# Optimization experiments

Hardware: AMD Instinct MI355X
Metric: run time of the kernel (lower is better)

Reference implementation:

```python
import jax, jax.numpy as jnp
import numpy as np

N = 100000          # nodes
E = 1600000         # directed edges
F_IN = 512          # num_features
H = 8               # heads
FH = 8              # per-head out channels
C = H * FH          # 64 hidden channels
HID = (2 * C) // 2  # 64, PyG JK lstm hidden size
NUM_CLASSES = 40
NEG_SLOPE = 0.2     # GATConv leaky relu slope


def setup_inputs() -> dict:
    key = jax.random.key(0)
    ks = jax.random.split(key, 24)
    s = 0.1
    inp = {
        "x": jax.random.normal(ks[0], (N, F_IN), jnp.float32),
        "edge_index": jax.random.randint(ks[1], (2, E), 0, N, jnp.int64)
        if jax.config.jax_enable_x64 else jax.random.randint(ks[1], (2, E), 0, N, jnp.int32),
        # GATConv 1
        "W1": jax.random.normal(ks[2], (F_IN, H * FH), jnp.float32) * s,
        "a1_src": jax.random.normal(ks[3], (H, FH), jnp.float32) * s,
        "a1_dst": jax.random.normal(ks[4], (H, FH), jnp.float32) * s,
        "b1": jnp.zeros((H * FH,), jnp.float32),
        # GATConv 2
        "W2": jax.random.normal(ks[5], (C, H * FH), jnp.float32) * s,
        "a2_src": jax.random.normal(ks[6], (H, FH), jnp.float32) * s,
        "a2_dst": jax.random.normal(ks[7], (H, FH), jnp.float32) * s,
        "b2": jnp.zeros((H * FH,), jnp.float32),
        # JK bidirectional LSTM (torch gate order i,f,g,o)
        "Wih_f": jax.random.normal(ks[8], (4 * HID, C), jnp.float32) * s,
        "Whh_f": jax.random.normal(ks[9], (4 * HID, HID), jnp.float32) * s,
        "bih_f": jnp.zeros((4 * HID,), jnp.float32),
        "bhh_f": jnp.zeros((4 * HID,), jnp.float32),
        "Wih_b": jax.random.normal(ks[10], (4 * HID, C), jnp.float32) * s,
        "Whh_b": jax.random.normal(ks[11], (4 * HID, HID), jnp.float32) * s,
        "bih_b": jnp.zeros((4 * HID,), jnp.float32),
        "bhh_b": jnp.zeros((4 * HID,), jnp.float32),
        # JK attention head
        "w_att": jax.random.normal(ks[12], (2 * HID,), jnp.float32) * s,
        "b_att": jnp.zeros((), jnp.float32),
        # output layer (bias=False)
        "W_out": jax.random.normal(ks[13], (NUM_CLASSES, C), jnp.float32) * s,
    }
    return inp


def gat_layer(x, src, dst, W, a_src, a_dst, b):
    n = x.shape[0]
    h = (x @ W).reshape(n, H, FH)                       # [N,H,FH]
    al_s = jnp.einsum('nhf,hf->nh', h, a_src)           # [N,H]
    al_d = jnp.einsum('nhf,hf->nh', h, a_dst)
    e = jax.nn.leaky_relu(al_s[src] + al_d[dst], NEG_SLOPE)  # [E',H]
    m = jax.ops.segment_max(e, dst, num_segments=n)     # segment softmax over dst
    ex = jnp.exp(e - m[dst])
    ssum = jax.ops.segment_sum(ex, dst, num_segments=n)
    alpha = ex / ssum[dst]                              # [E',H]
    out = jax.ops.segment_sum(h[src] * alpha[:, :, None], dst, num_segments=n)
    return out.reshape(n, H * FH) + b


def lstm_dir(xs, Wih, Whh, bih, bhh):
    # xs: [L, N, C] -> hs: [L, N, HID]
    n = xs.shape[1]

    def step(carry, xt):
        hprev, cprev = carry
        g = xt @ Wih.T + bih + hprev @ Whh.T + bhh
        i, f, gg, o = jnp.split(g, 4, axis=-1)
        c = jax.nn.sigmoid(f) * cprev + jax.nn.sigmoid(i) * jnp.tanh(gg)
        hh = jax.nn.sigmoid(o) * jnp.tanh(c)
        return (hh, c), hh

    init = (jnp.zeros((n, HID), xs.dtype), jnp.zeros((n, HID), xs.dtype))
    _, hs = jax.lax.scan(step, init, xs)
    return hs


def reference(x, edge_index, W1, a1_src, a1_dst, b1, W2, a2_src, a2_dst, b2,
              Wih_f, Whh_f, bih_f, bhh_f, Wih_b, Whh_b, bih_b, bhh_b,
              w_att, b_att, W_out):
    n = x.shape[0]
    loop = jnp.arange(n, dtype=edge_index.dtype)        # PyG add_self_loops
    src = jnp.concatenate([edge_index[0], loop])
    dst = jnp.concatenate([edge_index[1], loop])

    # eval mode: dropouts are identity
    x1 = jax.nn.elu(gat_layer(x, src, dst, W1, a1_src, a1_dst, b1))   # [N,64]
    x2 = gat_layer(x1, src, dst, W2, a2_src, a2_dst, b2)              # [N,64]

    xs = jnp.stack([x1, x2], axis=0)                    # [L=2, N, 64]
    h_f = lstm_dir(xs, Wih_f, Whh_f, bih_f, bhh_f)
    h_b = lstm_dir(xs[::-1], Wih_b, Whh_b, bih_b, bhh_b)[::-1]
    hcat = jnp.concatenate([h_f, h_b], axis=-1)         # [2, N, 128]

    att = jnp.einsum('lnk,k->ln', hcat, w_att) + b_att  # [2, N]
    alpha = jax.nn.softmax(att, axis=0)
    final = jnp.sum(xs * alpha[:, :, None], axis=0)     # [N, 64]

    return jax.nn.log_softmax(final @ W_out.T, axis=-1)
```

## Files before the change

### kernel.cpp

```cpp
#include <hip/hip_runtime.h>
#include <math.h>

#define F_IN 512
#define NCLS 40
#define BSH 7
#define BNODES (1 << BSH)
#define CH 16384

typedef __attribute__((ext_vector_type(8))) short bf16x8;
typedef __attribute__((ext_vector_type(4))) float f32x4;

__device__ __forceinline__ f32x4 mfma_bf16(bf16x8 a, bf16x8 b, f32x4 c){
  return __builtin_amdgcn_mfma_f32_16x16x32_bf16(a, b, c, 0, 0, 0);
}
__device__ __forceinline__ float fsigm(float x){ return 1.f/(1.f+__expf(-x)); }
__device__ __forceinline__ float ftanh(float x){ return 1.f - 2.f/(__expf(2.f*x)+1.f); }
__device__ __forceinline__ unsigned short f2bf(float f){
  unsigned u = __float_as_uint(f);
  return (unsigned short)((u + 0x7fffu + ((u>>16)&1u)) >> 16);
}
__device__ __forceinline__ float bf2f(unsigned short h){
  return __uint_as_float(((unsigned)h) << 16);
}
__device__ __forceinline__ unsigned cvtpk(float lo, float hi){
  unsigned r;
  asm("v_cvt_pk_bf16_f32 %0, %1, %2" : "=v"(r) : "v"(lo), "v"(hi));
  return r;
}

__global__ __launch_bounds__(256) void k_pcount(const int* __restrict__ ei, int e, int n,
                                                int nb, int* __restrict__ bhist){
  __shared__ int h[1024];
  int b = blockIdx.x, t = threadIdx.x;
  for (int i = t; i < nb; i += 256) h[i] = 0;
  __syncthreads();
  int tot = e + n;
  int base = b*CH;
  int lim = min(base + CH, tot);
  for (int i = base + t; i < lim; i += 256){
    int d = (i < e) ? ei[e + i] : (i - e);
    atomicAdd(&h[d >> BSH], 1);
  }
  __syncthreads();
  for (int i = t; i < nb; i += 256) bhist[(size_t)b*nb + i] = h[i];
}

__global__ __launch_bounds__(256) void k_pscan1(int* __restrict__ bhist, int nb, int B,
                                                int* __restrict__ bcnt){
  int i = blockIdx.x*256 + threadIdx.x;
  if (i >= nb) return;
  int run = 0;
  for (int b = 0; b < B; b++){
    int v = bhist[(size_t)b*nb + i];
    bhist[(size_t)b*nb + i] = run;
    run += v;
  }
  bcnt[i] = run;
}

__global__ __launch_bounds__(256) void k_pscan2(const int* __restrict__ bcnt, int nb, int tot,
                                                int* __restrict__ bbase,
                                                int* __restrict__ rowptr, int n){
  __shared__ int sb[256];
  __shared__ int carry;
  int t = threadIdx.x;
  if (t == 0) carry = 0;
  __syncthreads();
  for (int c0 = 0; c0 < nb; c0 += 256){
    int v = (c0 + t < nb) ? bcnt[c0 + t] : 0;
    sb[t] = v; __syncthreads();
    for (int off = 1; off < 256; off <<= 1){
      int u = (t >= off) ? sb[t-off] : 0; __syncthreads();
      sb[t] += u; __syncthreads();
    }
    if (c0 + t < nb) bbase[c0 + t] = carry + sb[t] - v;
    __syncthreads();
    if (t == 0) carry += sb[255];
    __syncthreads();
  }
  if (t == 0){ bbase[nb] = carry; rowptr[n] = tot; }
}

__global__ __launch_bounds__(256) void k_pscatter(const int* __restrict__ ei, int e, int n,
                                                  int nb, const int* __restrict__ bhist,
                                                  const int* __restrict__ bbase,
                                                  unsigned* __restrict__ bedges){
  __shared__ int cur[1024];
  int b = blockIdx.x, t = threadIdx.x;
  for (int i = t; i < nb; i += 256)
    cur[i] = bbase[i] + bhist[(size_t)b*nb + i];
  __syncthreads();
  int tot = e + n;
  int base = b*CH;
  int lim = min(base + CH, tot);
  for (int i = base + t; i < lim; i += 256){
    int s, d;
    if (i < e){ s = ei[i]; d = ei[e + i]; } else { s = i - e; d = s; }
    int pos = atomicAdd(&cur[d >> BSH], 1);
    bedges[pos] = (unsigned)s | ((unsigned)(d & (BNODES-1)) << 20);
  }
}

__global__ __launch_bounds__(256) void k_bbuild(const unsigned* __restrict__ bedges,
                                                const int* __restrict__ bbase,
                                                int* __restrict__ rowptr, int* __restrict__ col, int n){
  int b = blockIdx.x;
  int t = threadIdx.x;
  __shared__ int hist[BNODES];
  __shared__ int sc[BNODES];
  __shared__ int cur[BNODES];
  int beg = bbase[b], end = bbase[b+1];
  if (t < BNODES) hist[t] = 0;
  __syncthreads();
  for (int i = beg + t; i < end; i += 256)
    atomicAdd(&hist[bedges[i] >> 20], 1);
  __syncthreads();
  int v = (t < BNODES) ? hist[t] : 0;
  if (t < BNODES) sc[t] = v;
  __syncthreads();
  for (int off = 1; off < BNODES; off <<= 1){
    int u = (t >= off && t < BNODES) ? sc[t-off] : 0;
    __syncthreads();
    if (t < BNODES) sc[t] += u;
    __syncthreads();
  }
  if (t < BNODES){
    int excl = sc[t] - v;
    int node = (b << BSH) + t;
    if (node < n) rowptr[node] = beg + excl;
    cur[t] = excl;
  }
  __syncthreads();
  for (int i = beg + t; i < end; i += 256){
    unsigned pk = bedges[i];
    int pos = atomicAdd(&cur[pk >> 20], 1);
    col[beg + pos] = (int)(pk & 0xFFFFFu);
  }
}

__global__ __launch_bounds__(256) void k_prep(
    const float* __restrict__ W1, const float* __restrict__ W2,
    const float* __restrict__ Wihf, const float* __restrict__ Whhf,
    const float* __restrict__ Wihb, const float* __restrict__ Whhb,
    unsigned short* __restrict__ W1T, unsigned short* __restrict__ W2T,
    unsigned short* __restrict__ Wfx, unsigned short* __restrict__ Wfh,
    unsigned short* __restrict__ Wbx, unsigned short* __restrict__ Wbh)
{
  int i = blockIdx.x*256 + threadIdx.x;
  if (i < 32768){
    int k = i >> 6, c = i & 63;
    W1T[c*512 + k] = f2bf(W1[i]);
  } else if (i < 36864){
    int j = i - 32768; int k = j >> 6, c = j & 63;
    W2T[c*64 + k] = f2bf(W2[j]);
  } else if (i < 102400){
    int j = i - 36864;
    int which = j >> 14, o = j & 16383;
    const float* src = which==0 ? Wihf : which==1 ? Whhf : which==2 ? Wihb : Whhb;
    unsigned short* dst = which==0 ? Wfx : which==1 ? Wfh : which==2 ? Wbx : Wbh;
    dst[o] = f2bf(src[o]);
  }
}

__global__ __launch_bounds__(256, 2) void k_gemm512(
    const float* __restrict__ Xf, const unsigned short* __restrict__ WT,
    const float* __restrict__ as_, const float* __restrict__ ad_,
    unsigned short* __restrict__ Hb, unsigned short* __restrict__ alsb,
    float* __restrict__ ald, int n)
{
  __shared__ unsigned short xs[64*512];
  int t = threadIdx.x;
  int n0 = blockIdx.x*64;
  char* xsb = reinterpret_cast<char*>(xs);

  bool full = (n0 + 64 <= n);
  #pragma unroll
  for (int i = 0; i < 16; i++){
    int g  = i*256 + t;
    int row = g >> 6;
    int ck  = g & 63;
    const float* src = full ? (Xf + (size_t)(n0 + row)*512 + ck*8)
                            : (Xf + (size_t)min(n0 + row, n-1)*512 + ck*8);
    float4 u0 = reinterpret_cast<const float4*>(src)[0];
    float4 u1 = reinterpret_cast<const float4*>(src)[1];
    uint4 pk;
    pk.x = cvtpk(u0.x, u0.y);
    pk.y = cvtpk(u0.z, u0.w);
    pk.z = cvtpk(u1.x, u1.y);
    pk.w = cvtpk(u1.z, u1.w);
    int byte = row*1024 + ((ck*16) ^ ((row & 7) << 4));
    *reinterpret_cast<uint4*>(xsb + byte) = pk;
  }
  __syncthreads();

  int w = t >> 6, l = t & 63;
  int c = l & 15, kg = l >> 4;
  int row = w*16 + c;
  const unsigned short* wp0 = WT + (size_t)c*512 + kg*8;

  f32x4 acc[4];
  #pragma unroll
  for (int j = 0; j < 4; j++) acc[j] = (f32x4){0.f,0.f,0.f,0.f};

  #pragma unroll
  for (int kt = 0; kt < 16; ++kt){
    int colb = (kt*64 + kg*16) ^ ((row & 7) << 4);
    bf16x8 a = *reinterpret_cast<const bf16x8*>(xsb + row*1024 + colb);
    #pragma unroll
    for (int j = 0; j < 4; j++){
      bf16x8 b = *reinterpret_cast<const bf16x8*>(wp0 + j*8192 + kt*32);
      acc[j] = mfma_bf16(a, b, acc[j]);
    }
  }

  float asl[4], adl[4];
  #pragma unroll
  for (int j = 0; j < 4; j++){ asl[j] = as_[j*16 + c]; adl[j] = ad_[j*16 + c]; }
  #pragma unroll
  for (int j = 0; j < 4; j++){
    #pragma unroll
    for (int r = 0; r < 4; r++){
      int grow = n0 + w*16 + kg*4 + r;
      float v = acc[j][r];
      if (grow < n) Hb[(size_t)grow*64 + j*16 + c] = f2bf(v);
      float sv = v*asl[j];
      float dv = v*adl[j];
      sv += __shfl_xor(sv, 1, 64); sv += __shfl_xor(sv, 2, 64); sv += __shfl_xor(sv, 4, 64);
      dv += __shfl_xor(dv, 1, 64); dv += __shfl_xor(dv, 2, 64); dv += __shfl_xor(dv, 4, 64);
      if ((c & 7) == 0 && grow < n){
        int head = j*2 + (c >> 3);
        alsb[(size_t)grow*8 + head] = f2bf(sv);
        ald [(size_t)grow*8 + head] = dv;
      }
    }
  }
}

__global__ __launch_bounds__(256) void k_gemm64(
    const unsigned short* __restrict__ Xh, const unsigned short* __restrict__ WT,
    const float* __restrict__ as_, const float* __restrict__ ad_,
    unsigned short* __restrict__ Hb, unsigned short* __restrict__ alsb,
    float* __restrict__ ald, int n)
{
  int t = threadIdx.x;
  int w = t >> 6, l = t & 63;
  int c = l & 15, kg = l >> 4;
  int n0 = blockIdx.x*64 + w*16;
  int row = min(n0 + c, n-1);
  f32x4 acc[4];
  #pragma unroll
  for (int j = 0; j < 4; j++) acc[j] = (f32x4){0.f,0.f,0.f,0.f};

  #pragma unroll
  for (int kt = 0; kt < 2; ++kt){
    int ko = kt*32 + kg*8;
    bf16x8 a = *reinterpret_cast<const bf16x8*>(Xh + (size_t)row*64 + ko);
    #pragma unroll
    for (int j = 0; j < 4; j++){
      bf16x8 b = *reinterpret_cast<const bf16x8*>(WT + (size_t)(j*16 + c)*64 + ko);
      acc[j] = mfma_bf16(a, b, acc[j]);
    }
  }
  float asl[4], adl[4];
  #pragma unroll
  for (int j = 0; j < 4; j++){ asl[j] = as_[j*16 + c]; adl[j] = ad_[j*16 + c]; }
  #pragma unroll
  for (int j = 0; j < 4; j++){
    #pragma unroll
    for (int r = 0; r < 4; r++){
      int grow = n0 + kg*4 + r;
      float v = acc[j][r];
      if (grow < n) Hb[(size_t)grow*64 + j*16 + c] = f2bf(v);
      float sv = v*asl[j];
      float dv = v*adl[j];
      sv += __shfl_xor(sv, 1, 64); sv += __shfl_xor(sv, 2, 64); sv += __shfl_xor(sv, 4, 64);
      dv += __shfl_xor(dv, 1, 64); dv += __shfl_xor(dv, 2, 64); dv += __shfl_xor(dv, 4, 64);
      if ((c & 7) == 0 && grow < n){
        int head = j*2 + (c >> 3);
        alsb[(size_t)grow*8 + head] = f2bf(sv);
        ald [(size_t)grow*8 + head] = dv;
      }
    }
  }
}

struct EdgeBuf {
  float a0, a1, a2, a3;
  uint4 h0, h1, h2, h3;
};

__device__ __forceinline__ void loadEB(EdgeBuf& b, const int* __restrict__ col,
                                       int pos, int beg, int end,
                                       const unsigned short* __restrict__ ap,
                                       const unsigned short* __restrict__ Hp){
  int s0 = (pos   < end) ? col[pos]   : col[beg];
  int s1 = (pos+1 < end) ? col[pos+1] : s0;
  int s2 = (pos+2 < end) ? col[pos+2] : s0;
  int s3 = (pos+3 < end) ? col[pos+3] : s0;
  b.a0 = bf2f(ap[s0*8]); b.a1 = bf2f(ap[s1*8]);
  b.a2 = bf2f(ap[s2*8]); b.a3 = bf2f(ap[s3*8]);
  b.h0 = *reinterpret_cast<const uint4*>(Hp + (size_t)s0*64);
  b.h1 = *reinterpret_cast<const uint4*>(Hp + (size_t)s1*64);
  b.h2 = *reinterpret_cast<const uint4*>(Hp + (size_t)s2*64);
  b.h3 = *reinterpret_cast<const uint4*>(Hp + (size_t)s3*64);
}

__device__ __forceinline__ void acc8(float (&acc)[8], float xf, uint4 g){
  acc[0] = fmaf(xf, bf2f((unsigned short)g.x), acc[0]);
  acc[1] = fmaf(xf, bf2f((unsigned short)(g.x>>16)), acc[1]);
  acc[2] = fmaf(xf, bf2f((unsigned short)g.y), acc[2]);
  acc[3] = fmaf(xf, bf2f((unsigned short)(g.y>>16)), acc[3]);
  acc[4] = fmaf(xf, bf2f((unsigned short)g.z), acc[4]);
  acc[5] = fmaf(xf, bf2f((unsigned short)(g.z>>16)), acc[5]);
  acc[6] = fmaf(xf, bf2f((unsigned short)g.w), acc[6]);
  acc[7] = fmaf(xf, bf2f((unsigned short)(g.w>>16)), acc[7]);
}

__device__ __forceinline__ void computeEB(const EdgeBuf& b, int pos, int end, float adv,
                                          float& ssum, float (&acc)[8]){
  float e0 = b.a0 + adv; e0 = (e0>0.f)?e0:0.2f*e0;
  float e1 = b.a1 + adv; e1 = (e1>0.f)?e1:0.2f*e1;
  float e2 = b.a2 + adv; e2 = (e2>0.f)?e2:0.2f*e2;
  float e3 = b.a3 + adv; e3 = (e3>0.f)?e3:0.2f*e3;
  float x0 = __expf(e0);
  float x1 = (pos+1 < end) ? __expf(e1) : 0.f;
  float x2 = (pos+2 < end) ? __expf(e2) : 0.f;
  float x3 = (pos+3 < end) ? __expf(e3) : 0.f;
  ssum += (x0 + x1) + (x2 + x3);
  acc8(acc, x0, b.h0);
  acc8(acc, x1, b.h1);
  acc8(acc, x2, b.h2);
  acc8(acc, x3, b.h3);
}

template<bool DO_ELU>
__global__ __launch_bounds__(256) void k_agg(
    const int* __restrict__ rowptr, const int* __restrict__ col,
    const unsigned short* __restrict__ Hb, const unsigned short* __restrict__ alsb,
    const float* __restrict__ ald, const float* __restrict__ bias,
    unsigned short* __restrict__ outb, int n)
{
  int grp = threadIdx.x >> 3;
  int ln  = threadIdx.x & 7;
  int node = blockIdx.x*32 + grp;
  if (node >= n) return;
  float adv = ald[node*8 + ln];
  int beg = rowptr[node], end = rowptr[node+1];
  const unsigned short* Hp = Hb + ln*8;
  const unsigned short* ap = alsb + ln;

  float acc[8];
  #pragma unroll
  for (int q = 0; q < 8; q++) acc[q] = 0.f;
  float ssum = 0.f;

  EdgeBuf A, B;
  int p = beg;
  loadEB(A, col, p,   beg, end, ap, Hp);
  loadEB(B, col, p+4, beg, end, ap, Hp);
  while (true){
    computeEB(A, p, end, adv, ssum, acc);
    if (p + 8 < end) loadEB(A, col, p+8, beg, end, ap, Hp);
    p += 4;
    if (p >= end) break;
    computeEB(B, p, end, adv, ssum, acc);
    if (p + 8 < end) loadEB(B, col, p+8, beg, end, ap, Hp);
    p += 4;
    if (p >= end) break;
  }

  float inv = 1.f/ssum;
  ushort4 pk0, pk1;
  float o[8];
  #pragma unroll
  for (int q = 0; q < 8; q++){
    o[q] = acc[q]*inv + bias[ln*8 + q];
    if (DO_ELU) o[q] = (o[q] > 0.f) ? o[q] : (__expf(o[q]) - 1.f);
  }
  pk0.x = f2bf(o[0]); pk0.y = f2bf(o[1]); pk0.z = f2bf(o[2]); pk0.w = f2bf(o[3]);
  pk1.x = f2bf(o[4]); pk1.y = f2bf(o[5]); pk1.z = f2bf(o[6]); pk1.w = f2bf(o[7]);
  *reinterpret_cast<ushort4*>(outb + (size_t)node*64 + ln*8)     = pk0;
  *reinterpret_cast<ushort4*>(outb + (size_t)node*64 + ln*8 + 4) = pk1;
}

__global__ __launch_bounds__(256) void k_lstm(
    const unsigned short* __restrict__ X1b, const unsigned short* __restrict__ X2b,
    const unsigned short* __restrict__ Wfx, const unsigned short* __restrict__ Wfh,
    const unsigned short* __restrict__ Wbx, const unsigned short* __restrict__ Wbh,
    const float* __restrict__ bihf, const float* __restrict__ bhhf,
    const float* __restrict__ bihb, const float* __restrict__ bhhb,
    const float* __restrict__ watt,
    float* __restrict__ pf0, float* __restrict__ pf1,
    float* __restrict__ pb0, float* __restrict__ pb1, int n)
{
  int dir = blockIdx.y;
  const unsigned short* X0 = dir ? X2b : X1b;
  const unsigned short* X1 = dir ? X1b : X2b;
  const unsigned short* Wx = dir ? Wbx : Wfx;
  const unsigned short* Wh = dir ? Wbh : Wfh;
  const float* bi = dir ? bihb : bihf;
  const float* bh = dir ? bhhb : bhhf;
  const float* wa = watt + dir*64;
  float* po0 = dir ? pb0 : pf0;
  float* po1 = dir ? pb1 : pf1;

  __shared__ unsigned short hls[32][72];
  __shared__ float attp[2][4][32];

  int t = threadIdx.x;
  int w = t >> 6, l = t & 63;
  int c = l & 15, kg = l >> 4;
  int n0 = blockIdx.x*32;
  int r0 = min(n0 + c, n-1);
  int r1 = min(n0 + 16 + c, n-1);

  int hid = w*16 + c;
  float bs0 = bi[hid]       + bh[hid];
  float bs1 = bi[hid + 64]  + bh[hid + 64];
  float bs2 = bi[hid + 128] + bh[hid + 128];
  float bs3 = bi[hid + 192] + bh[hid + 192];
  float wav = wa[hid];

  f32x4 acc[2][4];
  #pragma unroll
  for (int m = 0; m < 2; m++)
    #pragma unroll
    for (int g = 0; g < 4; g++) acc[m][g] = (f32x4){0.f,0.f,0.f,0.f};

  #pragma unroll
  for (int kt = 0; kt < 2; ++kt){
    int ko = kt*32 + kg*8;
    bf16x8 a0 = *reinterpret_cast<const bf16x8*>(X0 + (size_t)r0*64 + ko);
    bf16x8 a1 = *reinterpret_cast<const bf16x8*>(X0 + (size_t)r1*64 + ko);
    #pragma unroll
    for (int g = 0; g < 4; g++){
      bf16x8 b = *reinterpret_cast<const bf16x8*>(Wx + (size_t)(g*64 + hid)*64 + ko);
      acc[0][g] = mfma_bf16(a0, b, acc[0][g]);
      acc[1][g] = mfma_bf16(a1, b, acc[1][g]);
    }
  }
  float creg[2][4];
  #pragma unroll
  for (int m = 0; m < 2; m++){
    #pragma unroll
    for (int r = 0; r < 4; r++){
      int rl = m*16 + kg*4 + r;
      float gi = acc[m][0][r] + bs0;
      float gg = acc[m][2][r] + bs2;
      float go = acc[m][3][r] + bs3;
      float cc = fsigm(gi)*ftanh(gg);
      float hh = fsigm(go)*ftanh(cc);
      creg[m][r] = cc;
      hls[rl][hid] = f2bf(hh);
      float s = hh*wav;
      s += __shfl_xor(s, 1, 16);
      s += __shfl_xor(s, 2, 16);
      s += __shfl_xor(s, 4, 16);
      s += __shfl_xor(s, 8, 16);
      if (c == 0) attp[0][w][rl] = s;
    }
  }
  __syncthreads();

  #pragma unroll
  for (int m = 0; m < 2; m++)
    #pragma unroll
    for (int g = 0; g < 4; g++) acc[m][g] = (f32x4){0.f,0.f,0.f,0.f};

  #pragma unroll
  for (int kt = 0; kt < 4; ++kt){
    int ko = (kt & 1)*32 + kg*8;
    bf16x8 a0, a1;
    if (kt < 2){
      a0 = *reinterpret_cast<const bf16x8*>(X1 + (size_t)r0*64 + ko);
      a1 = *reinterpret_cast<const bf16x8*>(X1 + (size_t)r1*64 + ko);
    } else {
      a0 = *reinterpret_cast<const bf16x8*>(&hls[c][ko]);
      a1 = *reinterpret_cast<const bf16x8*>(&hls[16 + c][ko]);
    }
    const unsigned short* Wp = (kt < 2) ? Wx : Wh;
    #pragma unroll
    for (int g = 0; g < 4; g++){
      bf16x8 b = *reinterpret_cast<const bf16x8*>(Wp + (size_t)(g*64 + hid)*64 + ko);
      acc[0][g] = mfma_bf16(a0, b, acc[0][g]);
      acc[1][g] = mfma_bf16(a1, b, acc[1][g]);
    }
  }
  #pragma unroll
  for (int m = 0; m < 2; m++){
    #pragma unroll
    for (int r = 0; r < 4; r++){
      int rl = m*16 + kg*4 + r;
      float gi = acc[m][0][r] + bs0;
      float gf = acc[m][1][r] + bs1;
      float gg = acc[m][2][r] + bs2;
      float go = acc[m][3][r] + bs3;
      float cc = fsigm(gf)*creg[m][r] + fsigm(gi)*ftanh(gg);
      float hh = fsigm(go)*ftanh(cc);
      float s = hh*wav;
      s += __shfl_xor(s, 1, 16);
      s += __shfl_xor(s, 2, 16);
      s += __shfl_xor(s, 4, 16);
      s += __shfl_xor(s, 8, 16);
      if (c == 0) attp[1][w][rl] = s;
    }
  }
  __syncthreads();
  if (t < 32){
    int grow = n0 + t;
    if (grow < n) po0[grow] = attp[0][0][t] + attp[0][1][t] + attp[0][2][t] + attp[0][3][t];
  } else if (t < 64){
    int rr = t - 32;
    int grow = n0 + rr;
    if (grow < n) po1[grow] = attp[1][0][rr] + attp[1][1][rr] + attp[1][2][rr] + attp[1][3][rr];
  }
}

__global__ __launch_bounds__(256) void k_final(
    const unsigned short* __restrict__ x1b, const unsigned short* __restrict__ x2b,
    const float* __restrict__ pf0, const float* __restrict__ pf1,
    const float* __restrict__ pb0, const float* __restrict__ pb1,
    const float* __restrict__ Wout, float* __restrict__ out, int n)
{
  __shared__ __align__(16) float ws[NCLS][68];
  __shared__ __align__(16) float fs[32][68];
  int t = threadIdx.x;
  for (int i = t; i < NCLS*64; i += 256)
    ws[i>>6][i&63] = Wout[i];

  int n0 = blockIdx.x*32;
  int nd = t >> 3, q8 = t & 7;
  int g = n0 + nd;
  int eb = q8*8;
  if (g < n){
    float att0 = pf0[g] + pb1[g];
    float att1 = pf1[g] + pb0[g];
    float a0 = 1.f/(1.f + __expf(att1 - att0));
    float a1 = 1.f - a0;
    uint4 p1 = *reinterpret_cast<const uint4*>(x1b + (size_t)g*64 + eb);
    uint4 p2 = *reinterpret_cast<const uint4*>(x2b + (size_t)g*64 + eb);
    const unsigned* u1 = (const unsigned*)&p1;
    const unsigned* u2 = (const unsigned*)&p2;
    #pragma unroll
    for (int q = 0; q < 4; q++){
      float v1l = bf2f((unsigned short)u1[q]), v1h = bf2f((unsigned short)(u1[q]>>16));
      float v2l = bf2f((unsigned short)u2[q]), v2h = bf2f((unsigned short)(u2[q]>>16));
      fs[nd][eb + q*2 + 0] = a0*v1l + a1*v2l;
      fs[nd][eb + q*2 + 1] = a0*v1h + a1*v2h;
    }
  } else {
    #pragma unroll
    for (int q = 0; q < 8; q++) fs[nd][eb+q] = 0.f;
  }
  __syncthreads();

  float lg[5] = {0.f,0.f,0.f,0.f,0.f};
  #pragma unroll
  for (int k4 = 0; k4 < 16; k4++){
    float4 f = *reinterpret_cast<const float4*>(&fs[nd][k4*4]);
    #pragma unroll
    for (int q = 0; q < 5; q++){
      int cc = q8 + 8*q;
      float4 wv = *reinterpret_cast<const float4*>(&ws[cc][k4*4]);
      lg[q] = fmaf(f.x, wv.x, lg[q]);
      lg[q] = fmaf(f.y, wv.y, lg[q]);
      lg[q] = fmaf(f.z, wv.z, lg[q]);
      lg[q] = fmaf(f.w, wv.w, lg[q]);
    }
  }
  float mx = lg[0];
  #pragma unroll
  for (int q = 1; q < 5; q++) mx = fmaxf(mx, lg[q]);
  #pragma unroll
  for (int mk = 1; mk < 8; mk <<= 1) mx = fmaxf(mx, __shfl_xor(mx, mk, 64));
  float se = 0.f;
  #pragma unroll
  for (int q = 0; q < 5; q++) se += __expf(lg[q] - mx);
  #pragma unroll
  for (int mk = 1; mk < 8; mk <<= 1) se += __shfl_xor(se, mk, 64);
  float lse = __logf(se);
  if (g < n){
    #pragma unroll
    for (int q = 0; q < 5; q++)
      out[(size_t)g*NCLS + q8 + 8*q] = lg[q] - mx - lse;
  }
}

extern "C" void kernel_launch(void* const* d_in, const int* in_sizes, int n_in,
                              void* d_out, int out_size, void* d_ws, size_t ws_size,
                              hipStream_t stream)
{
  const float* x    = (const float*)d_in[0];
  const int*   ei   = (const int*)d_in[1];
  const float* W1   = (const float*)d_in[2];
  const float* a1s  = (const float*)d_in[3];
  const float* a1d  = (const float*)d_in[4];
  const float* b1   = (const float*)d_in[5];
  const float* W2   = (const float*)d_in[6];
  const float* a2s  = (const float*)d_in[7];
  const float* a2d  = (const float*)d_in[8];
  const float* b2   = (const float*)d_in[9];
  const float* Wih_f= (const float*)d_in[10];
  const float* Whh_f= (const float*)d_in[11];
  const float* bih_f= (const float*)d_in[12];
  const float* bhh_f= (const float*)d_in[13];
  const float* Wih_b= (const float*)d_in[14];
  const float* Whh_b= (const float*)d_in[15];
  const float* bih_b= (const float*)d_in[16];
  const float* bhh_b= (const float*)d_in[17];
  const float* watt = (const float*)d_in[18];
  const float* Wout = (const float*)d_in[20];
  float* out = (float*)d_out;

  int n = in_sizes[0] / F_IN;
  int e = in_sizes[1] / 2;
  int nb = (n + BNODES - 1) >> BSH;
  int B  = (e + n + CH - 1) / CH;

  char* p = (char*)d_ws;
  auto alloc = [&](size_t b)->char*{ char* r = p; p += (b + 255) & ~(size_t)255; return r; };
  int* rowptr = (int*)alloc((size_t)(n+1)*4);
  int* colidx = (int*)alloc((size_t)(e+n)*4);
  unsigned* bedges = (unsigned*)alloc((size_t)(e+n)*4);
  int* bhist  = (int*)alloc((size_t)B*nb*4);
  int* bcnt   = (int*)alloc((size_t)(nb+1)*4);
  int* bbase  = (int*)alloc((size_t)(nb+1)*4);
  unsigned short* hbuf = (unsigned short*)alloc((size_t)n*64*2);
  unsigned short* alsb = (unsigned short*)alloc((size_t)n*8*2);
  float* ald  = (float*)alloc((size_t)n*8*4);
  unsigned short* x1b = (unsigned short*)alloc((size_t)n*64*2);
  unsigned short* x2b = (unsigned short*)alloc((size_t)n*64*2);
  float* pf0 = (float*)alloc((size_t)n*4);
  float* pf1 = (float*)alloc((size_t)n*4);
  float* pb0 = (float*)alloc((size_t)n*4);
  float* pb1 = (float*)alloc((size_t)n*4);
  unsigned short* W1T = (unsigned short*)alloc((size_t)64*512*2);
  unsigned short* W2T = (unsigned short*)alloc((size_t)64*64*2);
  unsigned short* Wfx = (unsigned short*)alloc((size_t)256*64*2);
  unsigned short* Wfh = (unsigned short*)alloc((size_t)256*64*2);
  unsigned short* Wbx = (unsigned short*)alloc((size_t)256*64*2);
  unsigned short* Wbh = (unsigned short*)alloc((size_t)256*64*2);

  k_pcount<<<B, 256, 0, stream>>>(ei, e, n, nb, bhist);
  k_pscan1<<<(nb+255)/256, 256, 0, stream>>>(bhist, nb, B, bcnt);
  k_pscan2<<<1, 256, 0, stream>>>(bcnt, nb, e+n, bbase, rowptr, n);
  k_pscatter<<<B, 256, 0, stream>>>(ei, e, n, nb, bhist, bbase, bedges);
  k_bbuild<<<nb, 256, 0, stream>>>(bedges, bbase, rowptr, colidx, n);

  k_prep<<<400, 256, 0, stream>>>(W1, W2, Wih_f, Whh_f, Wih_b, Whh_b,
                                  W1T, W2T, Wfx, Wfh, Wbx, Wbh);

  int gblk = (n + 63)/64;
  k_gemm512<<<gblk, 256, 0, stream>>>(x, W1T, a1s, a1d, hbuf, alsb, ald, n);
  k_agg<true ><<<(n+31)/32, 256, 0, stream>>>(rowptr, colidx, hbuf, alsb, ald, b1, x1b, n);
  k_gemm64<<<gblk, 256, 0, stream>>>(x1b, W2T, a2s, a2d, hbuf, alsb, ald, n);
  k_agg<false><<<(n+31)/32, 256, 0, stream>>>(rowptr, colidx, hbuf, alsb, ald, b2, x2b, n);

  dim3 lgrid((n + 31)/32, 2);
  k_lstm<<<lgrid, 256, 0, stream>>>(x1b, x2b, Wfx, Wfh, Wbx, Wbh,
                                    bih_f, bhh_f, bih_b, bhh_b,
                                    watt, pf0, pf1, pb0, pb1, n);

  k_final<<<(n+3)/4, 256, 0, stream>>>(x1b, x2b, pf0, pf1, pb0, pb1, Wout, out, n);
}
```

Before: 504.7 us.

## Stream x into LDS via direct global_load_lds and split attention-logit computation out

The first GEMM now uses 64-thread blocks of 16 rows that load fp32 x straight into swizzled LDS with global_load_lds. The bf16 conversion moves to the MFMA operand read, so the register round-trip and the large bf16 staging tile go away and occupancy should rise. The per-head attention logits (src/dst dot products) are removed from both GEMM epilogues and computed in a separate k_att kernel that rereads the bf16 H. This cuts shuffle-reduction work in the epilogues but adds two extra launches and an extra read of H, and the logits are now computed from bf16-rounded H rather than fp32 accumulators.

```diff
diff --git a/kernel.cpp b/kernel.cpp
--- a/kernel.cpp
+++ b/kernel.cpp
@@ -162,40 +162,31 @@
   }
 }
 
-__global__ __launch_bounds__(256, 2) void k_gemm512(
+__global__ __launch_bounds__(64) void k_gemm512(
     const float* __restrict__ Xf, const unsigned short* __restrict__ WT,
-    const float* __restrict__ as_, const float* __restrict__ ad_,
-    unsigned short* __restrict__ Hb, unsigned short* __restrict__ alsb,
-    float* __restrict__ ald, int n)
+    unsigned short* __restrict__ Hb, int n)
 {
-  __shared__ unsigned short xs[64*512];
-  int t = threadIdx.x;
-  int n0 = blockIdx.x*64;
-  char* xsb = reinterpret_cast<char*>(xs);
-
-  bool full = (n0 + 64 <= n);
-  #pragma unroll
-  for (int i = 0; i < 16; i++){
-    int g  = i*256 + t;
-    int row = g >> 6;
-    int ck  = g & 63;
-    const float* src = full ? (Xf + (size_t)(n0 + row)*512 + ck*8)
-                            : (Xf + (size_t)min(n0 + row, n-1)*512 + ck*8);
-    float4 u0 = reinterpret_cast<const float4*>(src)[0];
-    float4 u1 = reinterpret_cast<const float4*>(src)[1];
-    uint4 pk;
-    pk.x = cvtpk(u0.x, u0.y);
-    pk.y = cvtpk(u0.z, u0.w);
-    pk.z = cvtpk(u1.x, u1.y);
-    pk.w = cvtpk(u1.z, u1.w);
-    int byte = row*1024 + ((ck*16) ^ ((row & 7) << 4));
-    *reinterpret_cast<uint4*>(xsb + byte) = pk;
-  }
-  __syncthreads();
-
-  int w = t >> 6, l = t & 63;
+  __shared__ float xs[16*512];
+  int l = threadIdx.x;
+  int n0 = blockIdx.x*16;
+
+  #pragma unroll
+  for (int j = 0; j < 32; j++){
+    int r = j >> 1, h = j & 1;
+    int rg = min(n0 + r, n-1);
+    int sb = (l*16) ^ ((r & 7) << 4);
+    const float* g = Xf + (size_t)rg*512 + h*256 + (sb >> 2);
+    float* lds = xs + r*512 + h*256;
+    __builtin_amdgcn_global_load_lds(
+        (const __attribute__((address_space(1))) unsigned*)g,
+        (__attribute__((address_space(3))) unsigned*)lds, 16, 0, 0);
+  }
+  __syncthreads();
+
   int c = l & 15, kg = l >> 4;
-  int row = w*16 + c;
+  int r = c;
+  int xorr = (r & 7) << 4;
+  const char* xsb = reinterpret_cast<const char*>(xs);
   const unsigned short* wp0 = WT + (size_t)c*512 + kg*8;
 
   f32x4 acc[4];
@@ -204,43 +195,56 @@
 
   #pragma unroll
   for (int kt = 0; kt < 16; ++kt){
-    int colb = (kt*64 + kg*16) ^ ((row & 7) << 4);
-    bf16x8 a = *reinterpret_cast<const bf16x8*>(xsb + row*1024 + colb);
+    int b0 = (kt*128 + kg*32) ^ xorr;
+    int b1 = (kt*128 + kg*32 + 16) ^ xorr;
+    float4 u0 = *reinterpret_cast<const float4*>(xsb + (size_t)r*2048 + b0);
+    float4 u1 = *reinterpret_cast<const float4*>(xsb + (size_t)r*2048 + b1);
+    union { unsigned u[4]; bf16x8 v; } cc;
+    cc.u[0] = cvtpk(u0.x, u0.y);
+    cc.u[1] = cvtpk(u0.z, u0.w);
+    cc.u[2] = cvtpk(u1.x, u1.y);
+    cc.u[3] = cvtpk(u1.z, u1.w);
     #pragma unroll
     for (int j = 0; j < 4; j++){
       bf16x8 b = *reinterpret_cast<const bf16x8*>(wp0 + j*8192 + kt*32);
-      acc[j] = mfma_bf16(a, b, acc[j]);
-    }
-  }
-
-  float asl[4], adl[4];
-  #pragma unroll
-  for (int j = 0; j < 4; j++){ asl[j] = as_[j*16 + c]; adl[j] = ad_[j*16 + c]; }
+      acc[j] = mfma_bf16(cc.v, b, acc[j]);
+    }
+  }
+
   #pragma unroll
   for (int j = 0; j < 4; j++){
     #pragma unroll
-    for (int r = 0; r < 4; r++){
-      int grow = n0 + w*16 + kg*4 + r;
-      float v = acc[j][r];
-      if (grow < n) Hb[(size_t)grow*64 + j*16 + c] = f2bf(v);
-      float sv = v*asl[j];
-      float dv = v*adl[j];
-      sv += __shfl_xor(sv, 1, 64); sv += __shfl_xor(sv, 2, 64); sv += __shfl_xor(sv, 4, 64);
-      dv += __shfl_xor(dv, 1, 64); dv += __shfl_xor(dv, 2, 64); dv += __shfl_xor(dv, 4, 64);
-      if ((c & 7) == 0 && grow < n){
-        int head = j*2 + (c >> 3);
-        alsb[(size_t)grow*8 + head] = f2bf(sv);
-        ald [(size_t)grow*8 + head] = dv;
-      }
-    }
-  }
+    for (int rr = 0; rr < 4; rr++){
+      int grow = n0 + kg*4 + rr;
+      if (grow < n) Hb[(size_t)grow*64 + j*16 + c] = f2bf(acc[j][rr]);
+    }
+  }
+}
+
+__global__ void k_att(const unsigned short* __restrict__ Hb,
+                      const float* __restrict__ as_, const float* __restrict__ ad_,
+                      unsigned short* __restrict__ alsb, float* __restrict__ ald, int n){
+  int i = blockIdx.x*256 + threadIdx.x;
+  if (i >= n*8) return;
+  int head = i & 7;
+  uint4 pk = *reinterpret_cast<const uint4*>(Hb + (size_t)i*8);
+  float h[8];
+  h[0]=bf2f((unsigned short)pk.x); h[1]=bf2f((unsigned short)(pk.x>>16));
+  h[2]=bf2f((unsigned short)pk.y); h[3]=bf2f((unsigned short)(pk.y>>16));
+  h[4]=bf2f((unsigned short)pk.z); h[5]=bf2f((unsigned short)(pk.z>>16));
+  h[6]=bf2f((unsigned short)pk.w); h[7]=bf2f((unsigned short)(pk.w>>16));
+  float sv = 0.f, dv = 0.f;
+  #pragma unroll
+  for (int j = 0; j < 8; j++){
+    sv = fmaf(h[j], as_[head*8+j], sv);
+    dv = fmaf(h[j], ad_[head*8+j], dv);
+  }
+  alsb[i] = f2bf(sv); ald[i] = dv;
 }
 
 __global__ __launch_bounds__(256) void k_gemm64(
     const unsigned short* __restrict__ Xh, const unsigned short* __restrict__ WT,
-    const float* __restrict__ as_, const float* __restrict__ ad_,
-    unsigned short* __restrict__ Hb, unsigned short* __restrict__ alsb,
-    float* __restrict__ ald, int n)
+    unsigned short* __restrict__ Hb, int n)
 {
   int t = threadIdx.x;
   int w = t >> 6, l = t & 63;
@@ -261,25 +265,12 @@
       acc[j] = mfma_bf16(a, b, acc[j]);
     }
   }
-  float asl[4], adl[4];
-  #pragma unroll
-  for (int j = 0; j < 4; j++){ asl[j] = as_[j*16 + c]; adl[j] = ad_[j*16 + c]; }
   #pragma unroll
   for (int j = 0; j < 4; j++){
     #pragma unroll
-    for (int r = 0; r < 4; r++){
-      int grow = n0 + kg*4 + r;
-      float v = acc[j][r];
-      if (grow < n) Hb[(size_t)grow*64 + j*16 + c] = f2bf(v);
-      float sv = v*asl[j];
-      float dv = v*adl[j];
-      sv += __shfl_xor(sv, 1, 64); sv += __shfl_xor(sv, 2, 64); sv += __shfl_xor(sv, 4, 64);
-      dv += __shfl_xor(dv, 1, 64); dv += __shfl_xor(dv, 2, 64); dv += __shfl_xor(dv, 4, 64);
-      if ((c & 7) == 0 && grow < n){
-        int head = j*2 + (c >> 3);
-        alsb[(size_t)grow*8 + head] = f2bf(sv);
-        ald [(size_t)grow*8 + head] = dv;
-      }
+    for (int rr = 0; rr < 4; rr++){
+      int grow = n0 + kg*4 + rr;
+      if (grow < n) Hb[(size_t)grow*64 + j*16 + c] = f2bf(acc[j][rr]);
     }
   }
 }
@@ -650,10 +641,11 @@
   k_prep<<<400, 256, 0, stream>>>(W1, W2, Wih_f, Whh_f, Wih_b, Whh_b,
                                   W1T, W2T, Wfx, Wfh, Wbx, Wbh);
 
-  int gblk = (n + 63)/64;
-  k_gemm512<<<gblk, 256, 0, stream>>>(x, W1T, a1s, a1d, hbuf, alsb, ald, n);
+  k_gemm512<<<(n + 15)/16, 64, 0, stream>>>(x, W1T, hbuf, n);
+  k_att<<<(n*8+255)/256, 256, 0, stream>>>(hbuf, a1s, a1d, alsb, ald, n);
   k_agg<true ><<<(n+31)/32, 256, 0, stream>>>(rowptr, colidx, hbuf, alsb, ald, b1, x1b, n);
-  k_gemm64<<<gblk, 256, 0, stream>>>(x1b, W2T, a2s, a2d, hbuf, alsb, ald, n);
+  k_gemm64<<<(n + 63)/64, 256, 0, stream>>>(x1b, W2T, hbuf, n);
+  k_att<<<(n*8+255)/256, 256, 0, stream>>>(hbuf, a2s, a2d, alsb, ald, n);
   k_agg<false><<<(n+31)/32, 256, 0, stream>>>(rowptr, colidx, hbuf, alsb, ald, b2, x2b, n);
 
   dim3 lgrid((n + 31)/32, 2);
```

Measured after the change: 493.7 us, median of 2. -2.2%, faster.

## Make layer-1 GEMM persistent with double-buffered direct-to-LDS fp32 tile loads

Applied to the files above, without the earlier changes.

Rewrites k_gemm512 as a persistent kernel: 512 single-wave blocks each loop over 16-row tiles. Each block prefetches the next fp32 tile straight into LDS with global_load_lds while computing on the current one, and converts to bf16 when reading from LDS instead of converting before the LDS store. The aim is to overlap the dominant streaming read of x with the MFMA work and avoid the staging-through-registers plus block-wide barrier of the old version. In exchange, LDS holds fp32 (twice the footprint), and residency is limited to about two waves per CU, which may not keep enough memory traffic in flight.

```diff
diff --git a/kernel.cpp b/kernel.cpp
--- a/kernel.cpp
+++ b/kernel.cpp
@@ -162,77 +162,91 @@
   }
 }
 
-__global__ __launch_bounds__(256, 2) void k_gemm512(
+__global__ __launch_bounds__(64) void k_gemm512(
     const float* __restrict__ Xf, const unsigned short* __restrict__ WT,
     const float* __restrict__ as_, const float* __restrict__ ad_,
     unsigned short* __restrict__ Hb, unsigned short* __restrict__ alsb,
     float* __restrict__ ald, int n)
 {
-  __shared__ unsigned short xs[64*512];
-  int t = threadIdx.x;
-  int n0 = blockIdx.x*64;
-  char* xsb = reinterpret_cast<char*>(xs);
-
-  bool full = (n0 + 64 <= n);
-  #pragma unroll
-  for (int i = 0; i < 16; i++){
-    int g  = i*256 + t;
-    int row = g >> 6;
-    int ck  = g & 63;
-    const float* src = full ? (Xf + (size_t)(n0 + row)*512 + ck*8)
-                            : (Xf + (size_t)min(n0 + row, n-1)*512 + ck*8);
-    float4 u0 = reinterpret_cast<const float4*>(src)[0];
-    float4 u1 = reinterpret_cast<const float4*>(src)[1];
-    uint4 pk;
-    pk.x = cvtpk(u0.x, u0.y);
-    pk.y = cvtpk(u0.z, u0.w);
-    pk.z = cvtpk(u1.x, u1.y);
-    pk.w = cvtpk(u1.z, u1.w);
-    int byte = row*1024 + ((ck*16) ^ ((row & 7) << 4));
-    *reinterpret_cast<uint4*>(xsb + byte) = pk;
-  }
-  __syncthreads();
-
-  int w = t >> 6, l = t & 63;
+  __shared__ float xs[2][16*512];
+  int l = threadIdx.x;
   int c = l & 15, kg = l >> 4;
-  int row = w*16 + c;
+  int nt = (n + 15) >> 4;
+
+  auto stage = [&](int tile, int buf){
+    int n0t = tile << 4;
+    #pragma unroll
+    for (int j = 0; j < 32; j++){
+      int r = j >> 1, h = j & 1;
+      int rg = min(n0t + r, n-1);
+      int sb = (l*16) ^ ((r & 7) << 4);
+      const float* g = Xf + (size_t)rg*512 + h*256 + (sb >> 2);
+      float* lds = &xs[buf][0] + r*512 + h*256;
+      __builtin_amdgcn_global_load_lds(
+          (const __attribute__((address_space(1))) unsigned*)g,
+          (__attribute__((address_space(3))) unsigned*)lds, 16, 0, 0);
+    }
+  };
+
+  int tile = blockIdx.x;
+  if (tile >= nt) return;
+  stage(tile, 0);
+  int buf = 0;
+
+  float asl[4], adl[4];
+  #pragma unroll
+  for (int j = 0; j < 4; j++){ asl[j] = as_[j*16 + c]; adl[j] = ad_[j*16 + c]; }
   const unsigned short* wp0 = WT + (size_t)c*512 + kg*8;
-
-  f32x4 acc[4];
-  #pragma unroll
-  for (int j = 0; j < 4; j++) acc[j] = (f32x4){0.f,0.f,0.f,0.f};
-
-  #pragma unroll
-  for (int kt = 0; kt < 16; ++kt){
-    int colb = (kt*64 + kg*16) ^ ((row & 7) << 4);
-    bf16x8 a = *reinterpret_cast<const bf16x8*>(xsb + row*1024 + colb);
+  int xorr = (c & 7) << 4;
+
+  for (; tile < nt; tile += gridDim.x){
+    int nxt = tile + gridDim.x;
+    asm volatile("s_waitcnt vmcnt(0)" ::: "memory");
+    if (nxt < nt) stage(nxt, buf ^ 1);
+
+    const char* xsb = reinterpret_cast<const char*>(&xs[buf][0]);
+    f32x4 acc[4];
+    #pragma unroll
+    for (int j = 0; j < 4; j++) acc[j] = (f32x4){0.f,0.f,0.f,0.f};
+
+    #pragma unroll
+    for (int kt = 0; kt < 16; ++kt){
+      int b0 = (kt*128 + kg*32) ^ xorr;
+      int b1 = (kt*128 + kg*32 + 16) ^ xorr;
+      float4 u0 = *reinterpret_cast<const float4*>(xsb + (size_t)c*2048 + b0);
+      float4 u1 = *reinterpret_cast<const float4*>(xsb + (size_t)c*2048 + b1);
+      union { unsigned u[4]; bf16x8 v; } cc;
+      cc.u[0] = cvtpk(u0.x, u0.y);
+      cc.u[1] = cvtpk(u0.z, u0.w);
+      cc.u[2] = cvtpk(u1.x, u1.y);
+      cc.u[3] = cvtpk(u1.z, u1.w);
+      #pragma unroll
+      for (int j = 0; j < 4; j++){
+        bf16x8 b = *reinterpret_cast<const bf16x8*>(wp0 + j*8192 + kt*32);
+        acc[j] = mfma_bf16(cc.v, b, acc[j]);
+      }
+    }
+
+    int n0 = tile << 4;
     #pragma unroll
     for (int j = 0; j < 4; j++){
-      bf16x8 b = *reinterpret_cast<const bf16x8*>(wp0 + j*8192 + kt*32);
-      acc[j] = mfma_bf16(a, b, acc[j]);
-    }
-  }
-
-  float asl[4], adl[4];
-  #pragma unroll
-  for (int j = 0; j < 4; j++){ asl[j] = as_[j*16 + c]; adl[j] = ad_[j*16 + c]; }
-  #pragma unroll
-  for (int j = 0; j < 4; j++){
-    #pragma unroll
-    for (int r = 0; r < 4; r++){
-      int grow = n0 + w*16 + kg*4 + r;
-      float v = acc[j][r];
-      if (grow < n) Hb[(size_t)grow*64 + j*16 + c] = f2bf(v);
-      float sv = v*asl[j];
-      float dv = v*adl[j];
-      sv += __shfl_xor(sv, 1, 64); sv += __shfl_xor(sv, 2, 64); sv += __shfl_xor(sv, 4, 64);
-      dv += __shfl_xor(dv, 1, 64); dv += __shfl_xor(dv, 2, 64); dv += __shfl_xor(dv, 4, 64);
-      if ((c & 7) == 0 && grow < n){
-        int head = j*2 + (c >> 3);
-        alsb[(size_t)grow*8 + head] = f2bf(sv);
-        ald [(size_t)grow*8 + head] = dv;
+      #pragma unroll
+      for (int rr = 0; rr < 4; rr++){
+        int grow = n0 + kg*4 + rr;
+        float v = acc[j][rr];
+        if (grow < n) Hb[(size_t)grow*64 + j*16 + c] = f2bf(v);
+        float sv = v*asl[j];
+        float dv = v*adl[j];
+        sv += __shfl_xor(sv, 1, 64); sv += __shfl_xor(sv, 2, 64); sv += __shfl_xor(sv, 4, 64);
+        dv += __shfl_xor(dv, 1, 64); dv += __shfl_xor(dv, 2, 64); dv += __shfl_xor(dv, 4, 64);
+        if ((c & 7) == 0 && grow < n){
+          int head = j*2 + (c >> 3);
+          alsb[(size_t)grow*8 + head] = f2bf(sv);
+          ald [(size_t)grow*8 + head] = dv;
+        }
       }
     }
+    buf ^= 1;
   }
 }
 
@@ -267,9 +281,9 @@
   #pragma unroll
   for (int j = 0; j < 4; j++){
     #pragma unroll
-    for (int r = 0; r < 4; r++){
-      int grow = n0 + kg*4 + r;
-      float v = acc[j][r];
+    for (int rr = 0; rr < 4; rr++){
+      int grow = n0 + kg*4 + rr;
+      float v = acc[j][rr];
       if (grow < n) Hb[(size_t)grow*64 + j*16 + c] = f2bf(v);
       float sv = v*asl[j];
       float dv = v*adl[j];
@@ -650,10 +664,9 @@
   k_prep<<<400, 256, 0, stream>>>(W1, W2, Wih_f, Whh_f, Wih_b, Whh_b,
                                   W1T, W2T, Wfx, Wfh, Wbx, Wbh);
 
-  int gblk = (n + 63)/64;
-  k_gemm512<<<gblk, 256, 0, stream>>>(x, W1T, a1s, a1d, hbuf, alsb, ald, n);
+  k_gemm512<<<512, 64, 0, stream>>>(x, W1T, a1s, a1d, hbuf, alsb, ald, n);
   k_agg<true ><<<(n+31)/32, 256, 0, stream>>>(rowptr, colidx, hbuf, alsb, ald, b1, x1b, n);
-  k_gemm64<<<gblk, 256, 0, stream>>>(x1b, W2T, a2s, a2d, hbuf, alsb, ald, n);
+  k_gemm64<<<(n + 63)/64, 256, 0, stream>>>(x1b, W2T, a2s, a2d, hbuf, alsb, ald, n);
   k_agg<false><<<(n+31)/32, 256, 0, stream>>>(rowptr, colidx, hbuf, alsb, ald, b2, x2b, n);
 
   dim3 lgrid((n + 31)/32, 2);
```

After: 522.7 us (median of 4 runs). 3.6% more time.
